# Optimization experiments

Hardware: AMD Instinct MI355X
Metric: run time of the kernel (lower is better)

The kernel has to match this reference:

```python
import jax, jax.numpy as jnp
import numpy as np
from jax import lax

IN_CH, OUT_CH, K, STYLE_DIM = 512, 512, 3, 512
B, H, W = 16, 64, 64
SCALE = 1.0 / np.sqrt(IN_CH * K * K).astype(np.float32)
EPS = 1e-8


def setup_inputs() -> dict:
    key = jax.random.key(0)
    k1, k2, k3, k4 = jax.random.split(key, 4)
    return {
        "x": jax.random.normal(k1, (B, IN_CH, H, W), dtype=jnp.float32),
        "style": jax.random.normal(k2, (B, STYLE_DIM), dtype=jnp.float32),
        "weight": jax.random.normal(k3, (1, OUT_CH, IN_CH, K, K), dtype=jnp.float32),
        "mod_w": jax.random.normal(k4, (IN_CH, STYLE_DIM), dtype=jnp.float32) / np.sqrt(STYLE_DIM),
        "mod_b": jnp.ones((IN_CH,), dtype=jnp.float32),
    }


def reference(x, style, weight, mod_w, mod_b):
    b, cin, h, w = x.shape
    out_ch = weight.shape[1]
    k = weight.shape[-1]
    pad = k // 2
    # style projection: (B, in_channel)
    s = style @ mod_w.T + mod_b
    # modulated weight: (B, out, in, k, k)
    wmod = SCALE * weight * s[:, None, :, None, None]
    # demodulation: rsqrt of sum of squares over (in, kh, kw)
    demod = lax.rsqrt(jnp.sum(wmod * wmod, axis=(2, 3, 4)) + EPS)
    wmod = wmod * demod[:, :, None, None, None]
    # grouped conv with groups = batch
    wflat = wmod.reshape(b * out_ch, cin, k, k)
    xin = x.reshape(1, b * cin, h, w)
    out = lax.conv_general_dilated(
        xin, wflat,
        window_strides=(1, 1),
        padding=[(pad, pad), (pad, pad)],
        dimension_numbers=("NCHW", "OIHW", "NCHW"),
        feature_group_count=b,
    )
    return out.reshape(b, out_ch, h, w)
```

## Files before the change

kernel.cpp:

```cpp
#include <hip/hip_runtime.h>
#include <hip/hip_bf16.h>
#include <cstdint>
#include <cstddef>

typedef __bf16 bf16x8 __attribute__((ext_vector_type(8)));
typedef float f32x4 __attribute__((ext_vector_type(4)));
typedef float f32x16 __attribute__((ext_vector_type(16)));

#define MOD_SCALE 1.4731391e-02f
#define EPSF 1e-8f

__global__ __launch_bounds__(64) void k_style(
    const float* __restrict__ style, const float* __restrict__ mod_w,
    const float* __restrict__ mod_b, float* __restrict__ s)
{
  __shared__ float st[512];
  const int b = blockIdx.x >> 3, ig = blockIdx.x & 7;
  const int t = threadIdx.x;
  for (int k = t; k < 512; k += 64) st[k] = style[b*512 + k];
  __syncthreads();
  const int i = ig*64 + t;
  const float4* mw = (const float4*)(mod_w + (size_t)i*512);
  float acc = 0.f;
  #pragma unroll 8
  for (int j = 0; j < 128; ++j) {
    float4 v = mw[j];
    acc += v.x*st[4*j] + v.y*st[4*j+1] + v.z*st[4*j+2] + v.w*st[4*j+3];
  }
  s[b*512 + i] = acc + mod_b[i];
}

__global__ __launch_bounds__(256) void k_weight(
    const float* __restrict__ weight, float* __restrict__ w2,
    __hip_bfloat16* __restrict__ Wb)
{
  const int o = blockIdx.x, t = threadIdx.x;
  #pragma unroll
  for (int h = 0; h < 2; ++h) {
    const int i = t + h*256;
    const float* wp = weight + ((size_t)o*512 + i)*9;
    float sq = 0.f;
    #pragma unroll
    for (int kk = 0; kk < 9; ++kk) {
      float v = wp[kk];
      sq += v*v;
      Wb[((size_t)kk*512 + o)*512 + i] = __float2bfloat16(v * MOD_SCALE);
    }
    w2[(size_t)o*512 + i] = sq;
  }
}

__global__ __launch_bounds__(64) void k_demod(
    const float* __restrict__ s, const float* __restrict__ w2,
    float* __restrict__ demod)
{
  __shared__ float s2[512];
  const int b = blockIdx.x >> 3, og = blockIdx.x & 7;
  const int t = threadIdx.x;
  for (int k = t; k < 512; k += 64) { float a = s[b*512 + k]; s2[k] = a*a; }
  __syncthreads();
  const int o = og*64 + t;
  const float4* wp = (const float4*)(w2 + (size_t)o*512);
  float acc = 0.f;
  #pragma unroll 8
  for (int j = 0; j < 128; ++j) {
    float4 v = wp[j];
    acc += v.x*s2[4*j] + v.y*s2[4*j+1] + v.z*s2[4*j+2] + v.w*s2[4*j+3];
  }
  demod[b*512 + o] = rsqrtf(MOD_SCALE*MOD_SCALE*acc + EPSF);
}

__global__ __launch_bounds__(256) void k_xm(
    const float* __restrict__ x, const float* __restrict__ s,
    __hip_bfloat16* __restrict__ Xm)
{
  __shared__ __hip_bfloat16 T[64][72];
  const int bid = blockIdx.x;
  const int cb = bid & 7, y = (bid >> 3) & 63, b = bid >> 9;
  const int ic0 = cb*64;
  const int t = threadIdx.x;
  const int i = t >> 2;
  const int q = t & 3;
  const int x0 = q*16;
  const float sv = s[b*512 + ic0 + i];
  const float4* xp = (const float4*)(x + (size_t)(b*512 + ic0 + i)*4096 + y*64 + x0);
  float4 v[4] = {xp[0], xp[1], xp[2], xp[3]};
  __hip_bfloat16 tmp[16];
  #pragma unroll
  for (int j = 0; j < 4; ++j) {
    tmp[4*j+0] = __float2bfloat16(((const float*)&v[j])[0]*sv);
    tmp[4*j+1] = __float2bfloat16(((const float*)&v[j])[1]*sv);
    tmp[4*j+2] = __float2bfloat16(((const float*)&v[j])[2]*sv);
    tmp[4*j+3] = __float2bfloat16(((const float*)&v[j])[3]*sv);
  }
  *(float4*)&T[i][x0]     = *(const float4*)&tmp[0];
  *(float4*)&T[i][x0 + 8] = *(const float4*)&tmp[8];

  const float4 z4 = make_float4(0.f, 0.f, 0.f, 0.f);
  if (t < 16) {
    const int side = t >> 3, j = t & 7;
    float4* hz = (float4*)(Xm + (((size_t)(b*66 + (y+1))*66 + side*65)*512 + ic0 + j*8));
    *hz = z4;
  }
  if (y == 0) {
    for (int idx = t; idx < 528; idx += 256) {
      const int px = idx >> 3, j = idx & 7;
      float4* hz = (float4*)(Xm + (((size_t)(b*66 + 0)*66 + px)*512 + ic0 + j*8));
      *hz = z4;
    }
  }
  if (y == 63) {
    for (int idx = t; idx < 528; idx += 256) {
      const int px = idx >> 3, j = idx & 7;
      float4* hz = (float4*)(Xm + (((size_t)(b*66 + 65)*66 + px)*512 + ic0 + j*8));
      *hz = z4;
    }
  }

  __syncthreads();
  const int p = t >> 2;
  __hip_bfloat16 o16[16];
  #pragma unroll
  for (int cc = 0; cc < 16; ++cc) o16[cc] = T[q*16 + cc][p];
  __hip_bfloat16* dst = Xm + (((size_t)(b*66 + (y+1))*66 + (p+1))*512 + ic0 + q*16);
  *(float4*)dst       = *(const float4*)&o16[0];
  *(float4*)(dst + 8) = *(const float4*)&o16[8];
}

#define VMC(n) asm volatile("s_waitcnt vmcnt(" #n ")" ::: "memory")
#define LGKM0() do { \
    asm volatile("s_waitcnt lgkmcnt(0)" ::: "memory"); \
    __builtin_amdgcn_sched_barrier(0); \
  } while(0)

__global__ __launch_bounds__(512, 2) void k_conv(
    const __hip_bfloat16* __restrict__ Wb,
    const __hip_bfloat16* __restrict__ Xm,
    const float* __restrict__ demod,
    float* __restrict__ out)
{
  __shared__ __hip_bfloat16 lds[2][2][16384];

  const int orig = blockIdx.x;
  const int swz = (orig & 7)*64 + (orig >> 3);
  const int b  = swz >> 5;
  const int nt = (swz & 31) >> 1;
  const int mt = swz & 1;
  const int o0 = mt*256, y0 = nt*4;

  const int tid = threadIdx.x;
  const int l = tid & 63;
  const int w = tid >> 6;
  const int wm = w >> 2;
  const int wn = w & 3;

  const int srow = tid >> 3;
  const int tq   = (tid & 7) ^ (srow & 7);
  const char* WbC = (const char*)Wb;
  const char* XmC = (const char*)Xm;

  int aoff[2], boff[2], ldst[2];
  #pragma unroll
  for (int it = 0; it < 2; ++it) {
    const int R  = it*64 + srow;
    const int gr = (R & 0x6F) | ((tq & 1) << 4);
    const int gc = ((tq & 6) | ((R >> 4) & 1)) << 4;
    aoff[it] = (o0 + gr)*1024 + gc;
    boff[it] = (((b*66 + y0 + 1 + (gr >> 6))*66) + (gr & 63) + 1)*1024 + gc;
    ldst[it] = it*8192 + w*1024;
  }

  const int rowb = ((l >> 5) << 4) | (l & 15);
  const int lb4  = (l >> 4) & 1;
  const int sB   = (l & 7) << 4;

  #define STAGE_A(tau, h, bfi) do { \
    const int u_ = ((tau) >> 3)*524288 + (h)*131072 + (((tau) & 7) << 7); \
    _Pragma("unroll") \
    for (int it_ = 0; it_ < 2; ++it_) \
      __builtin_amdgcn_global_load_lds( \
        (__attribute__((address_space(1))) void*)(WbC + u_ + aoff[it_]), \
        (__attribute__((address_space(3))) void*)((char*)&lds[bfi][0][0] + (h)*16384 + ldst[it_]), \
        16, 0, 0); \
  } while(0)

  #define STAGE_B(tau, h, bfi) do { \
    const int kk_ = (tau) >> 3; \
    const int dy_ = kk_/3 - 1, dx_ = kk_ - (kk_/3)*3 - 1; \
    const int u_ = (((h)*2 + dy_)*66 + dx_)*1024 + (((tau) & 7) << 7); \
    _Pragma("unroll") \
    for (int it_ = 0; it_ < 2; ++it_) \
      __builtin_amdgcn_global_load_lds( \
        (__attribute__((address_space(1))) void*)(XmC + u_ + boff[it_]), \
        (__attribute__((address_space(3))) void*)((char*)&lds[bfi][1][0] + (h)*16384 + ldst[it_]), \
        16, 0, 0); \
  } while(0)

  #define RD_A(Ab, MH, dst) do { \
    _Pragma("unroll") \
    for (int mi_ = 0; mi_ < 2; ++mi_) \
      _Pragma("unroll") \
      for (int ks_ = 0; ks_ < 4; ++ks_) \
        dst[mi_][ks_] = *(const bf16x8*)((Ab) + (MH)*16384 + wm*8192 + mi_*4096 \
            + rowb*128 + (((((ks_<<1)|lb4)) << 4) ^ sB)); \
  } while(0)

  #define RD_B(Bb, NH, dst) do { \
    _Pragma("unroll") \
    for (int ks_ = 0; ks_ < 4; ++ks_) \
      dst[ks_] = *(const bf16x8*)((Bb) + (NH)*16384 + wn*4096 \
          + rowb*128 + (((((ks_<<1)|lb4)) << 4) ^ sB)); \
  } while(0)

  #define MFMAQ(AM0, dstA, NH, dstB) do { \
    _Pragma("unroll") \
    for (int ks_ = 0; ks_ < 4; ++ks_) \
      _Pragma("unroll") \
      for (int mi_ = 0; mi_ < 2; ++mi_) \
        acc[(AM0)+mi_][NH] = __builtin_amdgcn_mfma_f32_32x32x16_bf16( \
            dstA[mi_][ks_], dstB[ks_], acc[(AM0)+mi_][NH], 0, 0, 0); \
  } while(0)

  #define TILE(BFI, S1, S2, S3, S4, VM1, VM4) do { \
    const char* Ab_ = (const char*)&lds[BFI][0][0]; \
    const char* Bb_ = (const char*)&lds[BFI][1][0]; \
    bf16x8 a0_[2][4], a1_[2][4], b0_[4], b1_[4]; \
     \
    RD_A(Ab_, 0, a0_); RD_B(Bb_, 0, b0_); \
    S1; \
    __builtin_amdgcn_s_barrier(); \
    LGKM0(); \
    __builtin_amdgcn_s_setprio(1); MFMAQ(0, a0_, 0, b0_); __builtin_amdgcn_s_setprio(0); \
    VM1; \
    __builtin_amdgcn_s_barrier(); \
     \
    RD_B(Bb_, 1, b1_); \
    S2; \
    __builtin_amdgcn_s_barrier(); \
    LGKM0(); \
    __builtin_amdgcn_s_setprio(1); MFMAQ(0, a0_, 1, b1_); __builtin_amdgcn_s_setprio(0); \
    __builtin_amdgcn_s_barrier(); \
     \
    RD_A(Ab_, 1, a1_); \
    S3; \
    __builtin_amdgcn_s_barrier(); \
    LGKM0(); \
    __builtin_amdgcn_s_setprio(1); MFMAQ(2, a1_, 1, b1_); __builtin_amdgcn_s_setprio(0); \
    __builtin_amdgcn_s_barrier(); \
     \
    S4; \
    __builtin_amdgcn_s_barrier(); \
    __builtin_amdgcn_s_setprio(1); MFMAQ(2, a1_, 0, b0_); __builtin_amdgcn_s_setprio(0); \
    VM4; \
    __builtin_amdgcn_s_barrier(); \
  } while(0)

  f32x16 acc[4][2] = {};

  STAGE_A(0, 0, 0); STAGE_A(0, 1, 0); STAGE_B(0, 0, 0); STAGE_B(0, 1, 0);
  STAGE_B(1, 0, 1); STAGE_A(1, 1, 1);
  VMC(4);
  __builtin_amdgcn_s_barrier();

  #pragma unroll 1
  for (int tt = 0; tt < 35; ++tt) {
    const int t = tt*2;
    TILE(0, STAGE_A(t+1,0,1), STAGE_B(t+1,1,1), STAGE_B(t+2,0,0), STAGE_A(t+2,1,0),
            VMC(6), VMC(6));
    TILE(1, STAGE_A(t+2,0,0), STAGE_B(t+2,1,0), STAGE_B(t+3,0,1), STAGE_A(t+3,1,1),
            VMC(6), VMC(6));
  }
  TILE(0, STAGE_A(71,0,1), STAGE_B(71,1,1), (void)0, (void)0, VMC(6), VMC(2));
  TILE(1, (void)0, (void)0, (void)0, (void)0, VMC(0), (void)0);

  const int lr = l & 31;
  #pragma unroll
  for (int am = 0; am < 4; ++am) {
    const int om = o0 + (am >> 1)*128 + wm*64 + (am & 1)*32 + ((l >> 5) << 2);
    #pragma unroll
    for (int NH = 0; NH < 2; ++NH) {
      const int nc = NH*128 + wn*32 + lr;
      const int y = y0 + (nc >> 6), xx = nc & 63;
      #pragma unroll
      for (int g = 0; g < 4; ++g) {
        const f32x4 dm = *(const f32x4*)(demod + b*512 + om + 8*g);
        float* op = out + (size_t)(b*512 + om + 8*g)*4096 + y*64 + xx;
        #pragma unroll
        for (int j = 0; j < 4; ++j)
          op[(size_t)j*4096] = acc[am][NH][g*4 + j] * dm[j];
      }
    }
  }
  #undef TILE
  #undef MFMAQ
  #undef RD_A
  #undef RD_B
  #undef STAGE_A
  #undef STAGE_B
}

extern "C" void kernel_launch(void* const* d_in, const int* in_sizes, int n_in,
                              void* d_out, int out_size, void* d_ws, size_t ws_size,
                              hipStream_t stream)
{
  const float* x      = (const float*)d_in[0];
  const float* style  = (const float*)d_in[1];
  const float* weight = (const float*)d_in[2];
  const float* mod_w  = (const float*)d_in[3];
  const float* mod_b  = (const float*)d_in[4];
  float* out = (float*)d_out;

  char* ws = (char*)d_ws;
  float* s            = (float*)(ws);
  float* demod        = (float*)(ws + 32768);
  float* w2           = (float*)(ws + 65536);
  __hip_bfloat16* Wb  = (__hip_bfloat16*)(ws + 1114112);
  __hip_bfloat16* Xm  = (__hip_bfloat16*)(ws + 5832704);

  k_style <<<128,  64, 0, stream>>>(style, mod_w, mod_b, s);
  k_weight<<<512, 256, 0, stream>>>(weight, w2, Wb);
  k_demod <<<128,  64, 0, stream>>>(s, w2, demod);
  k_xm    <<<8192, 256, 0, stream>>>(x, s, Xm);
  k_conv  <<<512,  512, 0, stream>>>(Wb, Xm, demod, out);
}
```

Baseline: 353.9 us.

## Switch conv GEMM from 32x32x16 to 16x16x32 MFMA with simpler LDS layout

```diff
diff --git a/kernel.cpp b/kernel.cpp
--- a/kernel.cpp
+++ b/kernel.cpp
@@ -5,7 +5,6 @@
 
 typedef __bf16 bf16x8 __attribute__((ext_vector_type(8)));
 typedef float f32x4 __attribute__((ext_vector_type(4)));
-typedef float f32x16 __attribute__((ext_vector_type(16)));
 
 #define MOD_SCALE 1.4731391e-02f
 #define EPSF 1e-8f
@@ -155,24 +154,25 @@
   const int wn = w & 3;
 
   const int srow = tid >> 3;
-  const int tq   = (tid & 7) ^ (srow & 7);
+  const int scol = (((tid & 7) ^ (srow & 7)) << 4);
   const char* WbC = (const char*)Wb;
   const char* XmC = (const char*)Xm;
 
   int aoff[2], boff[2], ldst[2];
   #pragma unroll
   for (int it = 0; it < 2; ++it) {
-    const int R  = it*64 + srow;
-    const int gr = (R & 0x6F) | ((tq & 1) << 4);
-    const int gc = ((tq & 6) | ((R >> 4) & 1)) << 4;
-    aoff[it] = (o0 + gr)*1024 + gc;
-    boff[it] = (((b*66 + y0 + 1 + (gr >> 6))*66) + (gr & 63) + 1)*1024 + gc;
+    aoff[it] = (o0 + it*64 + srow)*1024 + scol;
+    boff[it] = (((b*66 + y0 + 1 + it)*66) + srow + 1)*1024 + scol;
     ldst[it] = it*8192 + w*1024;
   }
 
-  const int rowb = ((l >> 5) << 4) | (l & 15);
-  const int lb4  = (l >> 4) & 1;
+  const int frow = l & 15;
   const int sB   = (l & 7) << 4;
+  const int kq   = (l >> 4) << 4;
+  const int kc0  = (kq)      ^ sB;
+  const int kc1  = (64 | kq) ^ sB;
+  const int aBase = (wm*64 + frow)*128;
+  const int bBase = (wn*32 + frow)*128;
 
   #define STAGE_A(tau, h, bfi) do { \
     const int u_ = ((tau) >> 3)*524288 + (h)*131072 + (((tau) & 7) << 7); \
@@ -198,33 +198,35 @@
 
   #define RD_A(Ab, MH, dst) do { \
     _Pragma("unroll") \
-    for (int mi_ = 0; mi_ < 2; ++mi_) \
+    for (int mi_ = 0; mi_ < 4; ++mi_) { \
+      dst[mi_][0] = *(const bf16x8*)((Ab) + (MH)*16384 + aBase + mi_*2048 + kc0); \
+      dst[mi_][1] = *(const bf16x8*)((Ab) + (MH)*16384 + aBase + mi_*2048 + kc1); \
+    } \
+  } while(0)
+
+  #define RD_B(Bb, NH, dst) do { \
+    _Pragma("unroll") \
+    for (int ni_ = 0; ni_ < 2; ++ni_) { \
+      dst[ni_][0] = *(const bf16x8*)((Bb) + (NH)*16384 + bBase + ni_*2048 + kc0); \
+      dst[ni_][1] = *(const bf16x8*)((Bb) + (NH)*16384 + bBase + ni_*2048 + kc1); \
+    } \
+  } while(0)
+
+  #define MFMAQ(MH, dstA, NH, dstB) do { \
+    _Pragma("unroll") \
+    for (int ks_ = 0; ks_ < 2; ++ks_) \
       _Pragma("unroll") \
-      for (int ks_ = 0; ks_ < 4; ++ks_) \
-        dst[mi_][ks_] = *(const bf16x8*)((Ab) + (MH)*16384 + wm*8192 + mi_*4096 \
-            + rowb*128 + (((((ks_<<1)|lb4)) << 4) ^ sB)); \
-  } while(0)
-
-  #define RD_B(Bb, NH, dst) do { \
-    _Pragma("unroll") \
-    for (int ks_ = 0; ks_ < 4; ++ks_) \
-      dst[ks_] = *(const bf16x8*)((Bb) + (NH)*16384 + wn*4096 \
-          + rowb*128 + (((((ks_<<1)|lb4)) << 4) ^ sB)); \
-  } while(0)
-
-  #define MFMAQ(AM0, dstA, NH, dstB) do { \
-    _Pragma("unroll") \
-    for (int ks_ = 0; ks_ < 4; ++ks_) \
-      _Pragma("unroll") \
-      for (int mi_ = 0; mi_ < 2; ++mi_) \
-        acc[(AM0)+mi_][NH] = __builtin_amdgcn_mfma_f32_32x32x16_bf16( \
-            dstA[mi_][ks_], dstB[ks_], acc[(AM0)+mi_][NH], 0, 0, 0); \
+      for (int mi_ = 0; mi_ < 4; ++mi_) \
+        _Pragma("unroll") \
+        for (int ni_ = 0; ni_ < 2; ++ni_) \
+          acc[(MH)*4+mi_][(NH)*2+ni_] = __builtin_amdgcn_mfma_f32_16x16x32_bf16( \
+              dstA[mi_][ks_], dstB[ni_][ks_], acc[(MH)*4+mi_][(NH)*2+ni_], 0, 0, 0); \
   } while(0)
 
   #define TILE(BFI, S1, S2, S3, S4, VM1, VM4) do { \
     const char* Ab_ = (const char*)&lds[BFI][0][0]; \
     const char* Bb_ = (const char*)&lds[BFI][1][0]; \
-    bf16x8 a0_[2][4], a1_[2][4], b0_[4], b1_[4]; \
+    bf16x8 a0_[4][2], a1_[4][2], b0_[2][2], b1_[2][2]; \
      \
     RD_A(Ab_, 0, a0_); RD_B(Bb_, 0, b0_); \
     S1; \
@@ -245,17 +247,17 @@
     S3; \
     __builtin_amdgcn_s_barrier(); \
     LGKM0(); \
-    __builtin_amdgcn_s_setprio(1); MFMAQ(2, a1_, 1, b1_); __builtin_amdgcn_s_setprio(0); \
+    __builtin_amdgcn_s_setprio(1); MFMAQ(1, a1_, 1, b1_); __builtin_amdgcn_s_setprio(0); \
     __builtin_amdgcn_s_barrier(); \
      \
     S4; \
     __builtin_amdgcn_s_barrier(); \
-    __builtin_amdgcn_s_setprio(1); MFMAQ(2, a1_, 0, b0_); __builtin_amdgcn_s_setprio(0); \
+    __builtin_amdgcn_s_setprio(1); MFMAQ(1, a1_, 0, b0_); __builtin_amdgcn_s_setprio(0); \
     VM4; \
     __builtin_amdgcn_s_barrier(); \
   } while(0)
 
-  f32x16 acc[4][2] = {};
+  f32x4 acc[8][4] = {};
 
   STAGE_A(0, 0, 0); STAGE_A(0, 1, 0); STAGE_B(0, 0, 0); STAGE_B(0, 1, 0);
   STAGE_B(1, 0, 1); STAGE_A(1, 1, 1);
@@ -273,22 +275,18 @@
   TILE(0, STAGE_A(71,0,1), STAGE_B(71,1,1), (void)0, (void)0, VMC(6), VMC(2));
   TILE(1, (void)0, (void)0, (void)0, (void)0, VMC(0), (void)0);
 
-  const int lr = l & 31;
-  #pragma unroll
-  for (int am = 0; am < 4; ++am) {
-    const int om = o0 + (am >> 1)*128 + wm*64 + (am & 1)*32 + ((l >> 5) << 2);
+  #pragma unroll
+  for (int am = 0; am < 8; ++am) {
+    const int om = o0 + (am >> 2)*128 + wm*64 + (am & 3)*16 + ((l >> 4) << 2);
+    const f32x4 dm = *(const f32x4*)(demod + b*512 + om);
     #pragma unroll
-    for (int NH = 0; NH < 2; ++NH) {
-      const int nc = NH*128 + wn*32 + lr;
+    for (int nn = 0; nn < 4; ++nn) {
+      const int nc = (nn >> 1)*128 + wn*32 + (nn & 1)*16 + (l & 15);
       const int y = y0 + (nc >> 6), xx = nc & 63;
+      float* op = out + (size_t)(b*512 + om)*4096 + y*64 + xx;
       #pragma unroll
-      for (int g = 0; g < 4; ++g) {
-        const f32x4 dm = *(const f32x4*)(demod + b*512 + om + 8*g);
-        float* op = out + (size_t)(b*512 + om + 8*g)*4096 + y*64 + xx;
-        #pragma unroll
-        for (int j = 0; j < 4; ++j)
-          op[(size_t)j*4096] = acc[am][NH][g*4 + j] * dm[j];
-      }
+      for (int j = 0; j < 4; ++j)
+        op[(size_t)j*4096] = acc[am][nn][j] * dm[j];
     }
   }
   #undef TILE
```

After: 327.1 us, median of 2. 1.08x faster.
